# Performance work log

Hardware: AMD Instinct MI355X
Metric: run time of the kernel (lower is better)

## Reference

```python
import jax, jax.numpy as jnp
import numpy as np

N = 64
D_MODEL = 512
L_MAX = 2048
BATCH = 8
DT_MIN, DT_MAX = 1e-3, 1e-1


def _make_s4_buffers(n):
    r = np.arange(1, n + 1, dtype=np.float64)
    # hippo[i,j] = sqrt(2(i+1)+1)*sqrt(2(j+1)+1) if i>j, (i+1)+1 on diag, else 0
    hippo = np.where(r[:, None] > r[None, :],
                     np.sqrt(2 * r[:, None] + 1.0) * np.sqrt(2 * r[None, :] + 1.0),
                     0.0)
    hippo = hippo + np.diag(r + 1.0)
    nhippo = -hippo
    p = 0.5 * np.sqrt(2.0 * r + 1.0)
    q = 2.0 * p
    S = nhippo + p[:, None] * q[None, :]
    lmbda, V = np.linalg.eig(S)
    Vc = V.conj().T
    p = Vc @ p
    q = Vc @ q.conj()
    return (p.astype(np.complex64), q.astype(np.complex64), lmbda.astype(np.complex64))


def setup_inputs() -> dict:
    key = jax.random.key(0)
    ku, kb, kc, ks = jax.random.split(key, 4)
    u = jax.random.normal(ku, (BATCH, L_MAX, D_MODEL), dtype=jnp.float32)
    std = float(np.sqrt(2.0 / (N + D_MODEL)))  # xavier_normal for (n, d_model)
    B = jax.random.normal(kb, (D_MODEL, N), dtype=jnp.float32) * std
    Ct = jax.random.normal(kc, (D_MODEL, N), dtype=jnp.float32) * std
    D = jnp.ones((D_MODEL,), dtype=jnp.float32)
    scale = float(np.log(DT_MAX) - np.log(DT_MIN))
    log_step = jax.random.uniform(ks, (D_MODEL,), dtype=jnp.float32) * scale + float(np.log(DT_MIN))
    p, q, lmbda = _make_s4_buffers(N)
    omega_l = np.exp(2j * np.pi / L_MAX * np.arange(L_MAX)).astype(np.complex64)
    return {"u": u, "B": B, "Ct": Ct, "D": D, "log_step": log_step,
            "p": jnp.asarray(p), "q": jnp.asarray(q), "lmbda": jnp.asarray(lmbda),
            "omega_l": jnp.asarray(omega_l)}


def _s4_kernel(B, Ct, log_step, p, q, lmbda, omega_l):
    L = omega_l.shape[0]
    step = jnp.exp(log_step)                                   # [d]
    g = jnp.outer(2.0 / step, (1.0 - omega_l) / (1.0 + omega_l))  # [d, L] complex
    c = 2.0 / (1.0 + omega_l)                                  # [L]
    # shared Cauchy resolvent: 1/(g - lambda), [d, L, n]
    r = 1.0 / (g[:, :, None] - lmbda)
    a0 = jnp.conj(Ct)  # [d, n]
    a1 = jnp.conj(q)   # [n]
    k00 = jnp.einsum('dn,dln->dl', a0 * B, r)
    k01 = jnp.einsum('dn,dln->dl', a0 * p, r)
    k10 = jnp.einsum('dn,dln->dl', a1 * B, r)
    k11 = jnp.einsum('n,dln->dl', a1 * p, r)
    at_roots = c * (k00 - k01 * (1.0 / (1.0 + k11)) * k10)     # [d, L]
    Kf = jnp.fft.ifft(at_roots, n=L, axis=-1)
    order = (-jnp.arange(L)) % L                               # [0, L-1, ..., 1]
    return Kf[:, order].real                                   # [d, L] float32


def reference(u, B, Ct, D, log_step, p, q, lmbda, omega_l):
    L = u.shape[1]
    K = _s4_kernel(B, Ct, log_step, p, q, lmbda, omega_l)      # [d, L]
    # non-circular FFT convolution
    ud = jnp.fft.rfft(jnp.pad(u, ((0, 0), (0, L), (0, 0))), axis=1)   # [B, L+1, d]
    Kd = jnp.fft.rfft(jnp.pad(K, ((0, 0), (0, L))), axis=-1)          # [d, L+1]
    y = jnp.fft.irfft(ud.transpose(0, 2, 1) * Kd, axis=-1)[..., :L]   # [B, d, L]
    return y.transpose(0, 2, 1) + D[None, None, :] * u
```

## Files before the change

### kernel.cpp

```cpp
#include <hip/hip_runtime.h>
#include <hip/hip_bf16.h>

#define NT 256
#define R2f 0.70710678118654752f
#define CS1 0.92387953251128674f
#define SN1 0.38268343236508978f
#define PI2 6.2831853071795865f
#define LDSN 4336

__device__ __forceinline__ float2 cmulf(float2 a, float2 b) {
    return make_float2(a.x * b.x - a.y * b.y, a.x * b.y + a.y * b.x);
}
__device__ __forceinline__ float2 cadd(float2 a, float2 b) { return make_float2(a.x + b.x, a.y + b.y); }
__device__ __forceinline__ float2 csub(float2 a, float2 b) { return make_float2(a.x - b.x, a.y - b.y); }
__device__ __forceinline__ int padx(int i) { return i + ((i >> 8) << 4); }

template<bool INV>
__device__ __forceinline__ float2 tww(float2 v, float wx, float wy) {
    float sy = INV ? -wy : wy;
    return make_float2(v.x * wx - v.y * sy, v.x * sy + v.y * wx);
}
template<bool INV>
__device__ __forceinline__ float2 mul_mi(float2 v) {
    return INV ? make_float2(-v.y, v.x) : make_float2(v.y, -v.x);
}

template<bool INV>
__device__ __forceinline__ void dft4(float2& a, float2& b, float2& c, float2& d) {
    float2 t0 = cadd(a, c), t1 = csub(a, c);
    float2 t2 = cadd(b, d), t3 = csub(b, d);
    float2 jt3 = mul_mi<INV>(t3);
    a = cadd(t0, t2);
    c = csub(t0, t2);
    b = cadd(t1, jt3);
    d = csub(t1, jt3);
}

template<bool INV>
__device__ __forceinline__ void fft16_tail(float2 v[16]) {
    v[5]  = tww<INV>(v[5],  CS1, -SN1);
    v[9]  = tww<INV>(v[9],  R2f, -R2f);
    v[13] = tww<INV>(v[13], SN1, -CS1);
    v[6]  = tww<INV>(v[6],  R2f, -R2f);
    v[10] = mul_mi<INV>(v[10]);
    v[14] = tww<INV>(v[14], -R2f, -R2f);
    v[7]  = tww<INV>(v[7],  SN1, -CS1);
    v[11] = tww<INV>(v[11], -R2f, -R2f);
    v[15] = tww<INV>(v[15], -CS1,  SN1);
    dft4<INV>(v[0],  v[1],  v[2],  v[3]);
    dft4<INV>(v[4],  v[5],  v[6],  v[7]);
    dft4<INV>(v[8],  v[9],  v[10], v[11]);
    dft4<INV>(v[12], v[13], v[14], v[15]);
    float2 t;
    t = v[1];  v[1]  = v[4];  v[4]  = t;
    t = v[2];  v[2]  = v[8];  v[8]  = t;
    t = v[3];  v[3]  = v[12]; v[12] = t;
    t = v[6];  v[6]  = v[9];  v[9]  = t;
    t = v[7];  v[7]  = v[13]; v[13] = t;
    t = v[11]; v[11] = v[14]; v[14] = t;
}

template<bool INV>
__device__ __forceinline__ void fft16(float2 v[16]) {
    dft4<INV>(v[0], v[4], v[8],  v[12]);
    dft4<INV>(v[1], v[5], v[9],  v[13]);
    dft4<INV>(v[2], v[6], v[10], v[14]);
    dft4<INV>(v[3], v[7], v[11], v[15]);
    fft16_tail<INV>(v);
}

__device__ __forceinline__ void fft16_hz(float2 v[16]) {
    #pragma unroll
    for (int i = 0; i < 4; ++i) {
        float2 a = v[i], b = v[i + 4];
        float2 jb = make_float2(b.y, -b.x);
        v[i]      = cadd(a, b);
        v[i + 4]  = cadd(a, jb);
        v[i + 8]  = csub(a, b);
        v[i + 12] = csub(a, jb);
    }
    fft16_tail<false>(v);
}

template<bool INV>
__device__ __forceinline__ void twchain(float2 v[16], float ang) {
    float s, c;
    __sincosf(INV ? ang : -ang, &s, &c);
    float2 w = make_float2(c, s);
    float2 t = w;
    v[1] = cmulf(v[1], t);
    #pragma unroll
    for (int a = 2; a < 16; ++a) { t = cmulf(t, w); v[a] = cmulf(v[a], t); }
}

template<bool INV>
__device__ void fft4096(float2 v[16], float* ldsf, int tid) {
    const int hi = tid >> 4, lo = tid & 15;
    if (!INV) {
        fft16_hz(v);
        twchain<false>(v, PI2 * (float)tid * (1.0f / 4096.0f));
        __syncthreads();
        #pragma unroll
        for (int a = 0; a < 16; ++a) ldsf[padx(tid + 256 * a)] = v[a].x;
        __syncthreads();
        #pragma unroll
        for (int m1 = 0; m1 < 16; ++m1) v[m1].x = ldsf[padx(m1 * 16 + lo + 256 * hi)];
        __syncthreads();
        #pragma unroll
        for (int a = 0; a < 16; ++a) ldsf[padx(tid + 256 * a)] = v[a].y;
        __syncthreads();
        #pragma unroll
        for (int m1 = 0; m1 < 16; ++m1) v[m1].y = ldsf[padx(m1 * 16 + lo + 256 * hi)];
        fft16<false>(v);
        twchain<false>(v, PI2 * (float)lo * (1.0f / 256.0f));
        __syncthreads();
        #pragma unroll
        for (int b = 0; b < 16; ++b) ldsf[padx((lo + 16 * b + 256 * hi) ^ b)] = v[b].x;
        __syncthreads();
        #pragma unroll
        for (int m0 = 0; m0 < 16; ++m0) v[m0].x = ldsf[padx((m0 + 16 * lo + 256 * hi) ^ lo)];
        __syncthreads();
        #pragma unroll
        for (int b = 0; b < 16; ++b) ldsf[padx((lo + 16 * b + 256 * hi) ^ b)] = v[b].y;
        __syncthreads();
        #pragma unroll
        for (int m0 = 0; m0 < 16; ++m0) v[m0].y = ldsf[padx((m0 + 16 * lo + 256 * hi) ^ lo)];
        fft16<false>(v);
    } else {
        fft16<true>(v);
        __syncthreads();
        #pragma unroll
        for (int m0 = 0; m0 < 16; ++m0) ldsf[padx((m0 + 16 * lo + 256 * hi) ^ lo)] = v[m0].x;
        __syncthreads();
        #pragma unroll
        for (int b = 0; b < 16; ++b) v[b].x = ldsf[padx((lo + 16 * b + 256 * hi) ^ b)];
        __syncthreads();
        #pragma unroll
        for (int m0 = 0; m0 < 16; ++m0) ldsf[padx((m0 + 16 * lo + 256 * hi) ^ lo)] = v[m0].y;
        __syncthreads();
        #pragma unroll
        for (int b = 0; b < 16; ++b) v[b].y = ldsf[padx((lo + 16 * b + 256 * hi) ^ b)];
        twchain<true>(v, PI2 * (float)lo * (1.0f / 256.0f));
        fft16<true>(v);
        __syncthreads();
        #pragma unroll
        for (int m1 = 0; m1 < 16; ++m1) ldsf[padx(m1 * 16 + lo + 256 * hi)] = v[m1].x;
        __syncthreads();
        #pragma unroll
        for (int a = 0; a < 16; ++a) v[a].x = ldsf[padx(tid + 256 * a)];
        __syncthreads();
        #pragma unroll
        for (int m1 = 0; m1 < 16; ++m1) ldsf[padx(m1 * 16 + lo + 256 * hi)] = v[m1].y;
        __syncthreads();
        #pragma unroll
        for (int a = 0; a < 16; ++a) v[a].y = ldsf[padx(tid + 256 * a)];
        twchain<true>(v, PI2 * (float)tid * (1.0f / 4096.0f));
        fft16<true>(v);
    }
}

__global__ __launch_bounds__(256) void cauchy_kernel(
    const float* __restrict__ Bmat, const float* __restrict__ Ct,
    const float* __restrict__ log_step,
    const float2* __restrict__ p, const float2* __restrict__ q,
    const float2* __restrict__ lmbda, const float2* __restrict__ omega,
    float2* __restrict__ at)
{
    __shared__ float4 wA[64];
    __shared__ float4 wB[64];
    const int tid = threadIdx.x;
    const int d = blockIdx.x >> 2;
    const int lbase = (blockIdx.x & 3) << 8;

    if (tid < 64) {
        float b  = Bmat[d * 64 + tid];
        float ct = Ct[d * 64 + tid];
        float2 pp = p[tid], qq = q[tid];
        float2 lam = lmbda[tid];
        wA[tid] = make_float4(lam.x, lam.y, ct * b, qq.x * pp.x + qq.y * pp.y);
        wB[tid] = make_float4(ct * pp.x, ct * pp.y, b * qq.x, b * qq.y);
    }
    __syncthreads();

    const float two_over_dt = 2.0f * __expf(-log_step[d]);
    float2* atd = at + ((size_t)d << 11);

    const int l = lbase + tid;
    float2 om = omega[l];
    float dnx = 1.0f + om.x, dny = om.y;
    float id2 = __builtin_amdgcn_rcpf(dnx * dnx + dny * dny);
    float ivx = dnx * id2, ivy = -dny * id2;
    float ccx = 2.0f * ivx, ccy = 2.0f * ivy;
    float nmx = 1.0f - om.x, nmy = -om.y;
    float gx = two_over_dt * (nmx * ivx - nmy * ivy);
    float gy = two_over_dt * (nmx * ivy + nmy * ivx);

    float S00x = 0.f, S00y = 0.f, Sax = 0.f, Say = 0.f, Sbx = 0.f, Sby = 0.f;
    float Scx = 0.f, Scy = 0.f, Sdx = 0.f, Sdy = 0.f, S11x = 0.f, S11y = 0.f;

    #pragma unroll 8
    for (int n = 0; n < 64; ++n) {
        float4 A  = wA[n];
        float4 Bw = wB[n];
        float dx  = gx - A.x;
        float dy  = gy - A.y;
        float ir  = __builtin_amdgcn_rcpf(fmaf(dx, dx, dy * dy));
        float rx  = dx * ir;
        float ry  = -dy * ir;
        S00x = fmaf(A.z,  rx, S00x); S00y = fmaf(A.z,  ry, S00y);
        S11x = fmaf(A.w,  rx, S11x); S11y = fmaf(A.w,  ry, S11y);
        Sax  = fmaf(Bw.x, rx, Sax);  Say  = fmaf(Bw.x, ry, Say);
        Sbx  = fmaf(Bw.y, rx, Sbx);  Sby  = fmaf(Bw.y, ry, Sby);
        Scx  = fmaf(Bw.z, rx, Scx);  Scy  = fmaf(Bw.z, ry, Scy);
        Sdx  = fmaf(Bw.w, rx, Sdx);  Sdy  = fmaf(Bw.w, ry, Sdy);
    }

    {
        float k01x = Sax - Sby, k01y = Say + Sbx;
        float k10x = Scx + Sdy, k10y = Scy - Sdx;
        float ntx = k01x * k10x - k01y * k10y;
        float nty = k01x * k10y + k01y * k10x;
        float ox = 1.0f + S11x, oy = S11y;
        float oid = __builtin_amdgcn_rcpf(ox * ox + oy * oy);
        float tx = (ntx * ox + nty * oy) * oid;
        float ty = (nty * ox - ntx * oy) * oid;
        float inx = S00x - tx, iny = S00y - ty;
        float2 val = make_float2(ccx * inx - ccy * iny, ccx * iny + ccy * inx);
        atd[l] = val;
        if (l != 0) atd[2048 - l] = make_float2(val.x, -val.y);
    }

    if ((blockIdx.x & 3) == 3 && tid == 0) {
        float2 om1 = omega[1024];
        float dnx1 = 1.0f + om1.x, dny1 = om1.y;
        float id21 = __builtin_amdgcn_rcpf(dnx1 * dnx1 + dny1 * dny1);
        float ivx1 = dnx1 * id21, ivy1 = -dny1 * id21;
        float cx = 2.0f * ivx1, cy = 2.0f * ivy1;
        float nmx1 = 1.0f - om1.x, nmy1 = -om1.y;
        float ggx = two_over_dt * (nmx1 * ivx1 - nmy1 * ivy1);
        float ggy = two_over_dt * (nmx1 * ivy1 + nmy1 * ivx1);
        float s00x = 0.f, s00y = 0.f, sax = 0.f, say = 0.f, sbx = 0.f, sby = 0.f;
        float scx = 0.f, scy = 0.f, sdx = 0.f, sdy = 0.f, s11x = 0.f, s11y = 0.f;
        for (int n = 0; n < 64; ++n) {
            float4 A  = wA[n];
            float4 Bw = wB[n];
            float dx  = ggx - A.x;
            float dy  = ggy - A.y;
            float ir  = __builtin_amdgcn_rcpf(fmaf(dx, dx, dy * dy));
            float rx  = dx * ir;
            float ry  = -dy * ir;
            s00x = fmaf(A.z,  rx, s00x); s00y = fmaf(A.z,  ry, s00y);
            s11x = fmaf(A.w,  rx, s11x); s11y = fmaf(A.w,  ry, s11y);
            sax  = fmaf(Bw.x, rx, sax);  say  = fmaf(Bw.x, ry, say);
            sbx  = fmaf(Bw.y, rx, sbx);  sby  = fmaf(Bw.y, ry, sby);
            scx  = fmaf(Bw.z, rx, scx);  scy  = fmaf(Bw.z, ry, scy);
            sdx  = fmaf(Bw.w, rx, sdx);  sdy  = fmaf(Bw.w, ry, sdy);
        }
        float k01x = sax - sby, k01y = say + sbx;
        float k10x = scx + sdy, k10y = scy - sdx;
        float ntx = k01x * k10x - k01y * k10y;
        float nty = k01x * k10y + k01y * k10x;
        float ox = 1.0f + s11x, oy = s11y;
        float oid = __builtin_amdgcn_rcpf(ox * ox + oy * oy);
        float tx = (ntx * ox + nty * oy) * oid;
        float ty = (nty * ox - ntx * oy) * oid;
        float inx = s00x - tx, iny = s00y - ty;
        atd[1024] = make_float2(cx * inx - cy * iny, cx * iny + cy * inx);
    }
}

__global__ __launch_bounds__(256) void khat_kernel(
    const float2* __restrict__ at, float2* __restrict__ Khat)
{
    __shared__ float ldsf[LDSN];
    const int tid = threadIdx.x;
    const int d = blockIdx.x;
    const int hi = tid >> 4, lo = tid & 15;
    float2 v[16];

    const float2* ap = at + ((size_t)d << 11);
    #pragma unroll
    for (int n2 = 0; n2 < 8; ++n2) v[n2] = ap[tid + 256 * n2];
    #pragma unroll
    for (int n2 = 8; n2 < 16; ++n2) v[n2] = make_float2(0.f, 0.f);

    fft4096<false>(v, ldsf, tid);

    __syncthreads();
    if (!(hi & 1)) {
        int a2 = hi >> 1;
        #pragma unroll
        for (int c = 0; c < 16; ++c) {
            int j = 128 * c + 8 * lo + a2;
            ldsf[j ^ ((j >> 5) & 3)] = v[c].x * (1.0f / (2048.0f * 4096.0f));
        }
    }
    __syncthreads();
    #pragma unroll
    for (int n2 = 0; n2 < 8; ++n2) {
        int j = tid + 256 * n2;
        v[n2] = make_float2(ldsf[j ^ ((j >> 5) & 3)], 0.f);
    }
    #pragma unroll
    for (int n2 = 8; n2 < 16; ++n2) v[n2] = make_float2(0.f, 0.f);

    fft4096<false>(v, ldsf, tid);

    float2* op = Khat + ((size_t)d << 12);
    #pragma unroll
    for (int c = 0; c < 16; ++c) op[c * 256 + tid] = v[c];
}

__global__ __launch_bounds__(256) void transpose_pack_kernel(
    const float* __restrict__ u, float2* __restrict__ z)
{
    __shared__ float2 tile[64][33];
    const int tid = threadIdx.x;
    int sub = blockIdx.x;
    int lt = sub & 63;
    int dt = (sub >> 6) & 7;
    int bp = sub >> 9;
    const size_t ub0 = (size_t)(2 * bp) * 2048 * 512;
    const size_t ub1 = (size_t)(2 * bp + 1) * 2048 * 512;
    #pragma unroll
    for (int r = 0; r < 8; ++r) {
        int idx = tid + 256 * r;
        int l_in = idx >> 6;
        int d_in = idx & 63;
        size_t off = (size_t)(lt * 32 + l_in) * 512 + (dt * 64 + d_in);
        tile[d_in][l_in] = make_float2(u[ub0 + off], u[ub1 + off]);
    }
    __syncthreads();
    #pragma unroll
    for (int r = 0; r < 8; ++r) {
        int idx = tid + 256 * r;
        int d_out = idx >> 5;
        int l_out = idx & 31;
        z[((size_t)(bp * 512 + dt * 64 + d_out)) * 2048 + lt * 32 + l_out] = tile[d_out][l_out];
    }
}

__global__ __launch_bounds__(256) void conv_kernel(
    float2* __restrict__ z, const float2* __restrict__ Khat,
    const float* __restrict__ D)
{
    __shared__ float ldsf[LDSN];
    const int tid = threadIdx.x;
    const int d  = blockIdx.x & 511;
    const int bp = blockIdx.x >> 9;
    float2 v[16];
    float2 u0[8];

    float2* zr = z + ((size_t)(bp * 512 + d)) * 2048;
    #pragma unroll
    for (int n2 = 0; n2 < 8; ++n2) { u0[n2] = zr[tid + 256 * n2]; v[n2] = u0[n2]; }
    #pragma unroll
    for (int n2 = 8; n2 < 16; ++n2) v[n2] = make_float2(0.f, 0.f);

    fft4096<false>(v, ldsf, tid);

    const float2* kh = Khat + ((size_t)d << 12);
    #pragma unroll
    for (int c = 0; c < 16; ++c) v[c] = cmulf(v[c], kh[c * 256 + tid]);

    fft4096<true>(v, ldsf, tid);

    const float Dd = D[d];
    #pragma unroll
    for (int n2 = 0; n2 < 8; ++n2) {
        zr[tid + 256 * n2] =
            make_float2(v[n2].x + Dd * u0[n2].x, v[n2].y + Dd * u0[n2].y);
    }
}

__global__ __launch_bounds__(256) void untranspose_kernel(
    const float2* __restrict__ yz, float* __restrict__ out)
{
    __shared__ float2 tile[64][65];
    int blk = blockIdx.x;
    int lt  = blk & 31;
    int dt8 = (blk >> 5) & 7;
    int bp  = blk >> 8;
    for (int r = 0; r < 16; ++r) {
        int idx = threadIdx.x + 256 * r;
        int row = idx >> 6;
        int col = idx & 63;
        float2 vv = yz[((size_t)(bp * 512 + dt8 * 64 + row)) * 2048 + lt * 64 + col];
        tile[col][row] = vv;
    }
    __syncthreads();
    const size_t ub0 = (size_t)(2 * bp) * 2048 * 512;
    const size_t ub1 = (size_t)(2 * bp + 1) * 2048 * 512;
    for (int r = 0; r < 16; ++r) {
        int idx = threadIdx.x + 256 * r;
        int row = idx >> 6;
        int col = idx & 63;
        size_t off = (size_t)(lt * 64 + row) * 512 + (dt8 * 64 + col);
        float2 vv = tile[row][col];
        out[ub0 + off] = vv.x;
        out[ub1 + off] = vv.y;
    }
}

extern "C" void kernel_launch(void* const* d_in, const int* in_sizes, int n_in,
                              void* d_out, int out_size, void* d_ws, size_t ws_size,
                              hipStream_t stream) {
    (void)in_sizes; (void)n_in; (void)out_size; (void)ws_size;
    const float*  u   = (const float*)d_in[0];
    const float*  Bm  = (const float*)d_in[1];
    const float*  Ct  = (const float*)d_in[2];
    const float*  D   = (const float*)d_in[3];
    const float*  ls  = (const float*)d_in[4];
    const float2* p   = (const float2*)d_in[5];
    const float2* q   = (const float2*)d_in[6];
    const float2* lm  = (const float2*)d_in[7];
    const float2* om  = (const float2*)d_in[8];
    float* out = (float*)d_out;

    float2* Khat = (float2*)d_ws;
    float2* z    = (float2*)((char*)d_ws + (size_t)512 * 4096 * 8);
    float2* at   = z;

    hipLaunchKernelGGL(cauchy_kernel, dim3(2048), dim3(256), 0, stream,
                       Bm, Ct, ls, p, q, lm, om, at);
    hipLaunchKernelGGL(khat_kernel, dim3(512), dim3(256), 0, stream, at, Khat);
    hipLaunchKernelGGL(transpose_pack_kernel, dim3(2048), dim3(256), 0, stream, u, z);
    hipLaunchKernelGGL(conv_kernel, dim3(2048), dim3(256), 0, stream, z, Khat, D);
    hipLaunchKernelGGL(untranspose_kernel, dim3(1024), dim3(256), 0, stream, z, out);
}
```

Measured before the change: 86.94 us.

## Precompute Cauchy weight table in separate kernel and shrink untranspose tiles

Adds a small kernel that builds the per-channel Cauchy weight table in global memory once, so the cauchy kernel reads weights through uniform global loads instead of recomputing them in every block and synchronising on LDS. It also halves the untranspose tile to 64x32, doubling the grid to 2048 blocks for more parallelism and lower LDS use per block. The costs are an extra kernel launch, an extra workspace region, and global (cached) loads inside the hot loop in place of LDS reads.

```diff
diff --git a/kernel.cpp b/kernel.cpp
--- a/kernel.cpp
+++ b/kernel.cpp
@@ -159,28 +159,29 @@
     }
 }
 
+__global__ __launch_bounds__(256) void weights_kernel(
+    const float* __restrict__ Bmat, const float* __restrict__ Ct,
+    const float2* __restrict__ p, const float2* __restrict__ q,
+    const float2* __restrict__ lmbda, float4* __restrict__ wtab)
+{
+    int idx = blockIdx.x * 256 + threadIdx.x;
+    int d = idx >> 6, n = idx & 63;
+    float b  = Bmat[d * 64 + n];
+    float ct = Ct[d * 64 + n];
+    float2 pp = p[n], qq = q[n];
+    float2 lam = lmbda[n];
+    wtab[((size_t)d << 7) + 2 * n]     = make_float4(lam.x, lam.y, ct * b, qq.x * pp.x + qq.y * pp.y);
+    wtab[((size_t)d << 7) + 2 * n + 1] = make_float4(ct * pp.x, ct * pp.y, b * qq.x, b * qq.y);
+}
+
 __global__ __launch_bounds__(256) void cauchy_kernel(
-    const float* __restrict__ Bmat, const float* __restrict__ Ct,
-    const float* __restrict__ log_step,
-    const float2* __restrict__ p, const float2* __restrict__ q,
-    const float2* __restrict__ lmbda, const float2* __restrict__ omega,
-    float2* __restrict__ at)
-{
-    __shared__ float4 wA[64];
-    __shared__ float4 wB[64];
+    const float* __restrict__ log_step, const float2* __restrict__ omega,
+    const float4* __restrict__ wtab, float2* __restrict__ at)
+{
     const int tid = threadIdx.x;
     const int d = blockIdx.x >> 2;
     const int lbase = (blockIdx.x & 3) << 8;
-
-    if (tid < 64) {
-        float b  = Bmat[d * 64 + tid];
-        float ct = Ct[d * 64 + tid];
-        float2 pp = p[tid], qq = q[tid];
-        float2 lam = lmbda[tid];
-        wA[tid] = make_float4(lam.x, lam.y, ct * b, qq.x * pp.x + qq.y * pp.y);
-        wB[tid] = make_float4(ct * pp.x, ct * pp.y, b * qq.x, b * qq.y);
-    }
-    __syncthreads();
+    const float4* __restrict__ wd = wtab + ((size_t)d << 7);
 
     const float two_over_dt = 2.0f * __expf(-log_step[d]);
     float2* atd = at + ((size_t)d << 11);
@@ -200,8 +201,8 @@
 
     #pragma unroll 8
     for (int n = 0; n < 64; ++n) {
-        float4 A  = wA[n];
-        float4 Bw = wB[n];
+        float4 A  = wd[2 * n];
+        float4 Bw = wd[2 * n + 1];
         float dx  = gx - A.x;
         float dy  = gy - A.y;
         float ir  = __builtin_amdgcn_rcpf(fmaf(dx, dx, dy * dy));
@@ -242,8 +243,8 @@
         float s00x = 0.f, s00y = 0.f, sax = 0.f, say = 0.f, sbx = 0.f, sby = 0.f;
         float scx = 0.f, scy = 0.f, sdx = 0.f, sdy = 0.f, s11x = 0.f, s11y = 0.f;
         for (int n = 0; n < 64; ++n) {
-            float4 A  = wA[n];
-            float4 Bw = wB[n];
+            float4 A  = wd[2 * n];
+            float4 Bw = wd[2 * n + 1];
             float dx  = ggx - A.x;
             float dy  = ggy - A.y;
             float ir  = __builtin_amdgcn_rcpf(fmaf(dx, dx, dy * dy));
@@ -376,27 +377,29 @@
 __global__ __launch_bounds__(256) void untranspose_kernel(
     const float2* __restrict__ yz, float* __restrict__ out)
 {
-    __shared__ float2 tile[64][65];
-    int blk = blockIdx.x;
-    int lt  = blk & 31;
-    int dt8 = (blk >> 5) & 7;
-    int bp  = blk >> 8;
-    for (int r = 0; r < 16; ++r) {
-        int idx = threadIdx.x + 256 * r;
-        int row = idx >> 6;
-        int col = idx & 63;
-        float2 vv = yz[((size_t)(bp * 512 + dt8 * 64 + row)) * 2048 + lt * 64 + col];
-        tile[col][row] = vv;
+    __shared__ float2 tile[64][33];
+    const int tid = threadIdx.x;
+    int sub = blockIdx.x;
+    int lt = sub & 63;
+    int dt = (sub >> 6) & 7;
+    int bp = sub >> 9;
+    #pragma unroll
+    for (int r = 0; r < 8; ++r) {
+        int idx = tid + 256 * r;
+        int d_in = idx >> 5;
+        int l_in = idx & 31;
+        tile[d_in][l_in] = yz[((size_t)(bp * 512 + dt * 64 + d_in)) * 2048 + lt * 32 + l_in];
     }
     __syncthreads();
     const size_t ub0 = (size_t)(2 * bp) * 2048 * 512;
-    const size_t ub1 = (size_t)(2 * bp + 1) * 2048 * 512;
-    for (int r = 0; r < 16; ++r) {
-        int idx = threadIdx.x + 256 * r;
-        int row = idx >> 6;
-        int col = idx & 63;
-        size_t off = (size_t)(lt * 64 + row) * 512 + (dt8 * 64 + col);
-        float2 vv = tile[row][col];
+    const size_t ub1 = ub0 + (size_t)2048 * 512;
+    #pragma unroll
+    for (int r = 0; r < 8; ++r) {
+        int idx = tid + 256 * r;
+        int l_out = idx >> 6;
+        int d_out = idx & 63;
+        size_t off = (size_t)(lt * 32 + l_out) * 512 + dt * 64 + d_out;
+        float2 vv = tile[d_out][l_out];
         out[ub0 + off] = vv.x;
         out[ub1 + off] = vv.y;
     }
@@ -417,14 +420,20 @@
     const float2* om  = (const float2*)d_in[8];
     float* out = (float*)d_out;
 
+    const size_t KHAT_B = (size_t)512 * 4096 * sizeof(float2);
+    const size_t Z_B    = (size_t)2048 * 2048 * sizeof(float2);
+
     float2* Khat = (float2*)d_ws;
-    float2* z    = (float2*)((char*)d_ws + (size_t)512 * 4096 * 8);
+    float2* z    = (float2*)((char*)d_ws + KHAT_B);
     float2* at   = z;
-
+    float4* wtab = (float4*)((char*)d_ws + KHAT_B + Z_B);
+
+    hipLaunchKernelGGL(weights_kernel, dim3(128), dim3(256), 0, stream,
+                       Bm, Ct, p, q, lm, wtab);
     hipLaunchKernelGGL(cauchy_kernel, dim3(2048), dim3(256), 0, stream,
-                       Bm, Ct, ls, p, q, lm, om, at);
+                       ls, om, wtab, at);
     hipLaunchKernelGGL(khat_kernel, dim3(512), dim3(256), 0, stream, at, Khat);
     hipLaunchKernelGGL(transpose_pack_kernel, dim3(2048), dim3(256), 0, stream, u, z);
     hipLaunchKernelGGL(conv_kernel, dim3(2048), dim3(256), 0, stream, z, Khat, D);
-    hipLaunchKernelGGL(untranspose_kernel, dim3(1024), dim3(256), 0, stream, z, out);
-}
+    hipLaunchKernelGGL(untranspose_kernel, dim3(2048), dim3(256), 0, stream, z, out);
+}
```

Measured after the change: 91.19 us. 1.05x slower.
